# Optimization experiments

Measured on AMD Instinct MI355X. Metric: run time of the kernel, lower is better.

Reference implementation:

```python
import jax, jax.numpy as jnp
import numpy as np

H = 256           # hidden_size
S = 4             # num_subspaces
D = H // S        # subspace dim = 64
HD = 64           # mLSTM head_dim
EPS = 1e-8


def setup_inputs() -> dict:
    key = jax.random.key(0)
    ks = iter(jax.random.split(key, 40))
    def w(shape, scale=0.02):
        return (jax.random.normal(next(ks), shape, dtype=jnp.float32) * scale)
    B, T, Din = 256, 512, 128
    inp = {
        'x': jax.random.normal(next(ks), (B, T, Din), dtype=jnp.float32),
        # input projection
        'W_in': w((Din, H)), 'b_in': jnp.zeros((H,), jnp.float32),
        # layer 0: sLSTM (forget_bias buffer is zeros -> folded into b? keep explicit)
        's0_Wih': w((H, 4 * H)), 's0_bih': jnp.zeros((4 * H,), jnp.float32),
        's0_Whh': w((H, 4 * H)),
        # layer 1: mLSTM
        'm_Wq': w((H, HD)), 'm_bq': jnp.zeros((HD,), jnp.float32),
        'm_Wk': w((H, HD)), 'm_bk': jnp.zeros((HD,), jnp.float32),
        'm_Wv': w((H, HD)), 'm_bv': jnp.zeros((HD,), jnp.float32),
        'm_Wi': w((H, 1)), 'm_bi': jnp.zeros((1,), jnp.float32),
        'm_Wf': w((H, 1)), 'm_bf': jnp.zeros((1,), jnp.float32),
        'm_Wo': w((H, H)), 'm_bo': jnp.zeros((H,), jnp.float32),
        'm_Wp': w((HD, H)), 'm_bp': jnp.zeros((H,), jnp.float32),
        # subspace sLSTM cells (stacked over S); forget bias = -log(2^s)
        'sub_Wih': w((S, D, 4 * D)), 'sub_bih': jnp.zeros((S, 4 * D), jnp.float32),
        'sub_Whh': w((S, D, 4 * D)),
        'sub_fbias': jnp.asarray(-np.log(2.0 ** np.arange(S)), jnp.float32)[:, None] * jnp.ones((S, D), jnp.float32),
        # memory attention MLP
        'att_W1': w((D, D)), 'att_b1': jnp.zeros((D,), jnp.float32),
        'att_W2': w((D, 1)), 'att_b2': jnp.zeros((1,), jnp.float32),
        # layer norm
        'ln_g': jnp.ones((H,), jnp.float32), 'ln_b': jnp.zeros((H,), jnp.float32),
    }
    return inp


def _forward(x, W_in, b_in, s0_Wih, s0_bih, s0_Whh,
             m_Wq, m_bq, m_Wk, m_bk, m_Wv, m_bv, m_Wi, m_bi, m_Wf, m_bf,
             m_Wo, m_bo, m_Wp, m_bp,
             sub_Wih, sub_bih, sub_Whh, sub_fbias,
             att_W1, att_b1, att_W2, att_b2, ln_g, ln_b):
    B, T, _ = x.shape
    xh = x @ W_in + b_in                      # [B,T,H]
    xh = jnp.swapaxes(xh, 0, 1)               # [T,B,H] for scan

    def slstm(xt, h, c, n, Wih, bih, Whh, fbias):
        gates = xt @ Wih + bih + h @ Whh
        ig, fg, og, ct = jnp.split(gates, 4, axis=-1)
        i = jnp.exp(ig)
        f = jax.nn.sigmoid(fg + fbias)
        o = jax.nn.sigmoid(og)
        c_new = f * c + i * jnp.tanh(ct)
        n_new = f * n + i
        h_new = o * jnp.tanh(c_new / (n_new + EPS))
        return h_new, c_new, n_new

    def step(carry, xt):
        (h0, c0, n0, C1, n1, hs, cs, ns, _) = carry
        # layer 0: sLSTM, residual
        h0n, c0n, n0n = slstm(xt, h0, c0, n0, s0_Wih, s0_bih, s0_Whh, 0.0)
        x1 = h0n + xt
        # layer 1: mLSTM, residual
        q = x1 @ m_Wq + m_bq
        k = x1 @ m_Wk + m_bk
        v = x1 @ m_Wv + m_bv
        i1 = jnp.exp(x1 @ m_Wi + m_bi)              # [B,1]
        f1 = jax.nn.sigmoid(x1 @ m_Wf + m_bf)       # [B,1]
        C1n = f1[:, :, None] * C1 + i1[:, :, None] * (v[:, :, None] * k[:, None, :])
        n1n = f1 * n1 + i1                          # [B,1]
        Cq = jnp.einsum('bij,bj->bi', C1n, q)       # [B,HD]
        h_tilde = Cq / (n1n + EPS)
        o1 = jax.nn.sigmoid(x1 @ m_Wo + m_bo)
        h1n = o1 * jnp.tanh(h_tilde @ m_Wp + m_bp)
        x2 = h1n + x1
        # subspace sLSTM cells over S chunks (vectorized over s)
        xs = jnp.swapaxes(x2.reshape(B, S, D), 0, 1)   # [S,B,D]
        gates = (jnp.einsum('sbd,sdg->sbg', xs, sub_Wih) + sub_bih[:, None, :]
                 + jnp.einsum('sbd,sdg->sbg', hs, sub_Whh))
        ig, fg, og, ct = jnp.split(gates, 4, axis=-1)
        i = jnp.exp(ig)
        f = jax.nn.sigmoid(fg + sub_fbias[:, None, :])
        o = jax.nn.sigmoid(og)
        csn = f * cs + i * jnp.tanh(ct)
        nsn = f * ns + i
        hsn = o * jnp.tanh(csn / (nsn + EPS))          # [S,B,D]
        # attention fusion across subspaces
        score = jnp.tanh(hsn @ att_W1 + att_b1) @ att_W2 + att_b2  # [S,B,1]
        w = jax.nn.softmax(score[..., 0], axis=0)                  # [S,B]
        h_fused = jnp.sum(w[:, :, None] * hsn, axis=0)             # [B,D]
        h_final = jnp.tile(h_fused, (1, S))                        # [B,H]
        return (h0n, c0n, n0n, C1n, n1n, hsn, csn, nsn, h_final), None

    z = jnp.zeros
    carry0 = (z((B, H)), z((B, H)), jnp.ones((B, H)),
              z((B, HD, HD)), jnp.ones((B, 1)),
              z((S, B, D)), z((S, B, D)), jnp.ones((S, B, D)),
              z((B, H)))
    carryT, _ = jax.lax.scan(step, carry0, xh)
    out = carryT[-1]                                 # last-step h_final [B,H]
    mu = jnp.mean(out, axis=-1, keepdims=True)
    var = jnp.mean((out - mu) ** 2, axis=-1, keepdims=True)
    return (out - mu) / jnp.sqrt(var + 1e-5) * ln_g + ln_b


def reference(x, W_in, b_in, s0_Wih, s0_bih, s0_Whh,
              m_Wq, m_bq, m_Wk, m_bk, m_Wv, m_bv, m_Wi, m_bi, m_Wf, m_bf,
              m_Wo, m_bo, m_Wp, m_bp,
              sub_Wih, sub_bih, sub_Whh, sub_fbias,
              att_W1, att_b1, att_W2, att_b2, ln_g, ln_b):
    return _forward(x, W_in, b_in, s0_Wih, s0_bih, s0_Whh,
                    m_Wq, m_bq, m_Wk, m_bk, m_Wv, m_bv, m_Wi, m_bi, m_Wf, m_bf,
                    m_Wo, m_bo, m_Wp, m_bp,
                    sub_Wih, sub_bih, sub_Whh, sub_fbias,
                    att_W1, att_b1, att_W2, att_b2, ln_g, ln_b)
```

## Files before the change

### kernel.cpp

```cpp
#include <hip/hip_runtime.h>
#include <math.h>

#define TSTEPS 512
#define CH 16
#define NCHUNK 32
#define EPSR 1e-8f

#define OHH   0u
#define OSUB  262144u
#define OQK   393216u
#define OV    425984u
#define OWO   442368u
#define OWP   507904u
#define OWIN  524288u
#define NPACK1 557056u
#define OWC   557056u
#define OBC   688128u

typedef __fp16 h2_t __attribute__((ext_vector_type(2)));

__device__ __forceinline__ float dot2(unsigned int w, unsigned int a, float acc) {
    union U { unsigned int u; h2_t h; };
    U cw; cw.u = w; U ca; ca.u = a;
    return __builtin_amdgcn_fdot2(cw.h, ca.h, acc, false);
}
__device__ __forceinline__ unsigned int pk2f(float a, float b) {
    union { h2_t h; unsigned int u; } c;
    c.h = __builtin_amdgcn_cvt_pkrtz(a, b);
    return c.u;
}
__device__ __forceinline__ float bfu(unsigned int v) {
    union { unsigned int i; float f; } c; c.i = v; return c.f;
}
__device__ __forceinline__ float sigmoidf_(float v) { return 1.0f / (1.0f + expf(-v)); }
__device__ __forceinline__ unsigned short f2bf(float f) {
    unsigned int u = __float_as_uint(f);
    return (unsigned short)((u + 0x7fffu + ((u >> 16) & 1u)) >> 16);
}

extern "C" __global__ void pack_w(const float* __restrict__ Whh,
    const float* __restrict__ sWih, const float* __restrict__ sWhh,
    const float* __restrict__ Wq, const float* __restrict__ Wk, const float* __restrict__ Wv,
    const float* __restrict__ Wo, const float* __restrict__ Wp,
    const float* __restrict__ W_in, unsigned short* __restrict__ ws)
{
    unsigned e = blockIdx.x * 256u + threadIdx.x;
    if (e >= NPACK1) return;
    float v; bool isbf = false;
    if (e < OSUB) {
        unsigned idx = e >> 3, sl = e & 7u;
        unsigned jp = idx >> 8, t = idx & 255u, g = sl >> 1, ee = sl & 1u;
        v = Whh[(2u * jp + ee) * 1024u + g * 256u + t];
    } else if (e < OQK) {
        unsigned r = e - OSUB, idx = r >> 3, sl = r & 7u;
        unsigned q4 = idx & 3u, d = (idx >> 2) & 63u, jq = (idx >> 8) & 15u, s = idx >> 12;
        unsigned g = sl >> 1, ee = sl & 1u;
        unsigned j = jq * 4u + (q4 & 1u) * 2u + ee;
        const float* src = (q4 >> 1) ? sWhh : sWih;
        v = src[(s * 64u + j) * 256u + g * 64u + d];
    } else if (e < OV) {
        unsigned r = e - OQK, idx = r >> 3, sl = r & 7u;
        unsigned d = idx & 63u, jq = idx >> 6;
        unsigned j = jq * 4u + (sl & 3u);
        v = ((sl >> 2) ? Wk : Wq)[j * 64u + d];
    } else if (e < OWO) {
        unsigned r = e - OV, idx = r >> 2;
        unsigned d = idx & 63u, jq = idx >> 6, j = jq * 4u + (r & 3u);
        v = Wv[j * 64u + d];
    } else if (e < OWP) {
        unsigned r = e - OWO, idx = r >> 2;
        unsigned t = idx & 255u, jq = idx >> 8, j = jq * 4u + (r & 3u);
        v = Wo[j * 256u + t];
    } else if (e < OWIN) {
        unsigned r = e - OWP, idx = r >> 2;
        unsigned t = idx & 255u, jq = idx >> 8, j = jq * 4u + (r & 3u);
        v = Wp[j * 256u + t];
    } else {
        v = W_in[e - OWIN]; isbf = true;
    }
    if (isbf) ws[e] = f2bf(v);
    else { union { __fp16 h; unsigned short s; } c; c.h = (__fp16)v; ws[e] = c.s; }
}

extern "C" __global__ void compute_wc(const float* __restrict__ W_in,
    const float* __restrict__ Wih, const float* __restrict__ b_in,
    const float* __restrict__ bih, unsigned short* __restrict__ ws)
{
    unsigned e = blockIdx.x * 256u + threadIdx.x;
    if (e < 131072u) {
        unsigned k = e >> 10, n = e & 1023u;
        float acc = 0.f;
        for (int j = 0; j < 256; ++j) acc += W_in[k * 256 + j] * Wih[j * 1024 + n];
        unsigned t = n & 255u, g = n >> 8;
        ws[OWC + k * 1024 + t * 4 + g] = f2bf(acc);
    } else if (e < 132096u) {
        unsigned n = e - 131072u;
        float acc = bih[n];
        for (int j = 0; j < 256; ++j) acc += b_in[j] * Wih[j * 1024 + n];
        float* bc = (float*)(ws + OBC);
        bc[n] = acc;
    }
}

extern "C" __global__ __launch_bounds__(512)
void xlstm_seq(const float* __restrict__ x, const float* __restrict__ b_in,
               const float* __restrict__ bq, const float* __restrict__ bk, const float* __restrict__ bv,
               const float* __restrict__ Wi, const float* __restrict__ bi,
               const float* __restrict__ Wf, const float* __restrict__ bf,
               const float* __restrict__ bo, const float* __restrict__ bp,
               const float* __restrict__ sbih, const float* __restrict__ sfb,
               const float* __restrict__ aW1, const float* __restrict__ ab1,
               const float* __restrict__ aW2, const float* __restrict__ ab2,
               const float* __restrict__ lng, const float* __restrict__ lnb,
               const unsigned short* __restrict__ pk,
               float* __restrict__ out)
{
    const int u = threadIdx.x;
    const int b = blockIdx.x;
    const int t256 = u & 255;
    const int half = u >> 8;

    __shared__ float g_chunk[CH][1024];
    __shared__ float xt_chunk[CH][256];
    __shared__ __align__(16) float xT[128][20];
    __shared__ __align__(16) float x1_l[256], hs_l[256];
    __shared__ float opre_l[256];
    __shared__ float psum[4][520];
    __shared__ float qb[64], kb[64], vb[64];
    __shared__ float Cm[64 * 65];
    __shared__ float sc_l[16];
    __shared__ __align__(16) float Wi_l[256], Wf_l[256];
    __shared__ float sbih_l[1024], bc_l[1024];
    __shared__ float b_in_l[256], bo_l[256], bp_l[256], sfb_l[256], bqkv_l[192];
    __shared__ __align__(16) unsigned int h0p[128], x1p[128], x2p[128], hsp[128], htp[32];

    {
        const float* bcg = (const float*)(pk + OBC);
        for (int e = u; e < 1024; e += 512) { sbih_l[e] = sbih[e]; bc_l[e] = bcg[e]; }
    }
    if (u < 256) {
        Wi_l[u] = Wi[u]; Wf_l[u] = Wf[u];
        b_in_l[u] = b_in[u]; bo_l[u] = bo[u]; bp_l[u] = bp[u]; sfb_l[u] = sfb[u];
        hs_l[u] = 0.f;
    }
    if (u < 192) bqkv_l[u] = (u < 64) ? bq[u] : (u < 128) ? bk[u - 64] : bv[u - 128];
    if (u < 128) { h0p[u] = 0u; hsp[u] = 0u; }
    if (u == 0) { sc_l[10] = bi[0]; sc_l[11] = bf[0]; }
    for (int e = u; e < 64 * 65; e += 512) Cm[e] = 0.f;
    float c0 = 0.f, n0 = 1.f, cs = 0.f, ns = 1.f, n1 = 1.f;
    __syncthreads();

    const uint4* pwhh = reinterpret_cast<const uint4*>(pk + OHH) + t256;
    const uint4* psub = reinterpret_cast<const uint4*>(pk + OSUB)
                        + ((size_t)((t256 >> 6) * 1024 + (t256 & 63))) * 4;
    const uint4* pqk = reinterpret_cast<const uint4*>(pk + OQK) + (u & 63);
    const uint2* pv_ = reinterpret_cast<const uint2*>(pk + OV) + (u & 63);
    const uint2* pwo = reinterpret_cast<const uint2*>(pk + OWO) + t256;
    const uint2* pwp = reinterpret_cast<const uint2*>(pk + OWP) + t256;
    const unsigned short* pwin = pk + OWIN + t256;
    const uint2* pwc = reinterpret_cast<const uint2*>(pk + OWC) + t256;
    const float* xrow = x + (size_t)b * TSTEPS * 128;

    for (int cc = 0; cc < NCHUNK; ++cc) {
        {
            float4 xv4 = *reinterpret_cast<const float4*>(xrow + cc * (CH * 128) + u * 4);
            int m = u >> 5, k0 = (u * 4) & 127;
            xT[k0][m] = xv4.x; xT[k0 + 1][m] = xv4.y; xT[k0 + 2][m] = xv4.z; xT[k0 + 3][m] = xv4.w;
        }
        __syncthreads();

        {
            const int m0 = half * 8;
            float xtacc[8], gacc[4][8];
            {
                float bi_ = b_in_l[t256];
                #pragma unroll
                for (int e = 0; e < 8; ++e) xtacc[e] = bi_;
                #pragma unroll
                for (int g = 0; g < 4; ++g) {
                    float bcv = bc_l[g * 256 + t256];
                    #pragma unroll
                    for (int e = 0; e < 8; ++e) gacc[g][e] = bcv;
                }
            }
            #pragma unroll 4
            for (int k = 0; k < 128; ++k) {
                float wv = bfu((unsigned)pwin[k * 256] << 16);
                uint2 wg = pwc[k * 256];
                float w0 = bfu(wg.x << 16), w1 = bfu(wg.x & 0xffff0000u);
                float w2 = bfu(wg.y << 16), w3 = bfu(wg.y & 0xffff0000u);
                float4 a  = *reinterpret_cast<const float4*>(&xT[k][m0]);
                float4 b4 = *reinterpret_cast<const float4*>(&xT[k][m0 + 4]);
                #pragma unroll
                for (int e = 0; e < 8; ++e) {
                    float xv = (e == 0) ? a.x : (e == 1) ? a.y : (e == 2) ? a.z : (e == 3) ? a.w
                             : (e == 4) ? b4.x : (e == 5) ? b4.y : (e == 6) ? b4.z : b4.w;
                    xtacc[e]   += xv * wv;
                    gacc[0][e] += xv * w0;
                    gacc[1][e] += xv * w1;
                    gacc[2][e] += xv * w2;
                    gacc[3][e] += xv * w3;
                }
            }
            #pragma unroll
            for (int e = 0; e < 8; ++e) {
                xt_chunk[m0 + e][t256] = xtacc[e];
                g_chunk[m0 + e][t256]       = gacc[0][e];
                g_chunk[m0 + e][256 + t256] = gacc[1][e];
                g_chunk[m0 + e][512 + t256] = gacc[2][e];
                g_chunk[m0 + e][768 + t256] = gacc[3][e];
            }
        }
        __syncthreads();

        for (int st = 0; st < CH; ++st) {
            {
                float g0 = 0.f, g1 = 0.f, g2 = 0.f, g3 = 0.f;
                const int jp0 = half * 64;
                #pragma unroll 4
                for (int q = 0; q < 16; ++q) {
                    uint4 hp4 = *reinterpret_cast<const uint4*>(&h0p[jp0 + q * 4]);
                    #pragma unroll
                    for (int e = 0; e < 4; ++e) {
                        uint4 wk = pwhh[(size_t)(jp0 + q * 4 + e) * 256];
                        unsigned int hp = (e == 0) ? hp4.x : (e == 1) ? hp4.y : (e == 2) ? hp4.z : hp4.w;
                        g0 = dot2(wk.x, hp, g0);
                        g1 = dot2(wk.y, hp, g1);
                        g2 = dot2(wk.z, hp, g2);
                        g3 = dot2(wk.w, hp, g3);
                    }
                }
                psum[0][u] = g0; psum[1][u] = g1; psum[2][u] = g2; psum[3][u] = g3;
            }
            __syncthreads();
            if (u < 256) {
                float G0 = g_chunk[st][u]       + psum[0][u] + psum[0][256 + u];
                float G1 = g_chunk[st][256 + u] + psum[1][u] + psum[1][256 + u];
                float G2 = g_chunk[st][512 + u] + psum[2][u] + psum[2][256 + u];
                float G3 = g_chunk[st][768 + u] + psum[3][u] + psum[3][256 + u];
                float i0 = expf(G0), f0 = sigmoidf_(G1), o0 = sigmoidf_(G2);
                float cn = f0 * c0 + i0 * tanhf(G3);
                float nn = f0 * n0 + i0;
                c0 = cn; n0 = nn;
                float h0n = o0 * tanhf(cn / (nn + EPSR));
                float x1v = h0n + xt_chunk[st][u];
                x1_l[u] = x1v;
                float h0o = __shfl_xor(h0n, 1);
                float x1o = __shfl_xor(x1v, 1);
                if (!(u & 1)) { h0p[u >> 1] = pk2f(h0n, h0o); x1p[u >> 1] = pk2f(x1v, x1o); }
            }
            __syncthreads();

            if (u < 256) {
                const int jq0 = (u >> 6) * 16;
                float pq = 0.f, pkk = 0.f, pvv = 0.f;
                #pragma unroll 4
                for (int q = 0; q < 16; ++q) {
                    int jq = jq0 + q;
                    uint4 wqk = pqk[(size_t)jq * 64];
                    uint2 wv2 = pv_[(size_t)jq * 64];
                    uint2 ap = *reinterpret_cast<const uint2*>(&x1p[jq * 2]);
                    pq  = dot2(wqk.x, ap.x, pq);  pq  = dot2(wqk.y, ap.y, pq);
                    pkk = dot2(wqk.z, ap.x, pkk); pkk = dot2(wqk.w, ap.y, pkk);
                    pvv = dot2(wv2.x, ap.x, pvv); pvv = dot2(wv2.y, ap.y, pvv);
                }
                psum[0][u] = pq; psum[1][u] = pkk; psum[2][u] = pvv;
            } else if (u < 384) {
                const float* Wl = (u < 320) ? Wi_l : Wf_l;
                int j0 = (u & 63) * 4;
                float4 xv = *reinterpret_cast<const float4*>(&x1_l[j0]);
                float4 wv = *reinterpret_cast<const float4*>(&Wl[j0]);
                float p = xv.x * wv.x + xv.y * wv.y + xv.z * wv.z + xv.w * wv.w;
                #pragma unroll
                for (int off = 32; off > 0; off >>= 1) p += __shfl_down(p, off);
                if ((u & 63) == 0) sc_l[(u < 320) ? 8 : 9] = p;
            }
            __syncthreads();
            {
                int lane = u & 63;
                if (u < 64)        qb[u]    = bqkv_l[u]          + psum[0][u] + psum[0][64 + u] + psum[0][128 + u] + psum[0][192 + u];
                else if (u < 128)  kb[lane] = bqkv_l[64 + lane]  + psum[1][lane] + psum[1][64 + lane] + psum[1][128 + lane] + psum[1][192 + lane];
                else if (u < 192)  vb[lane] = bqkv_l[128 + lane] + psum[2][lane] + psum[2][64 + lane] + psum[2][128 + lane] + psum[2][192 + lane];
                else if (u == 192) sc_l[0] = expf(sc_l[10] + sc_l[8]);
                else if (u == 193) sc_l[1] = sigmoidf_(sc_l[11] + sc_l[9]);
            }
            __syncthreads();

            float i1 = sc_l[0], f1 = sc_l[1];
            n1 = f1 * n1 + i1;
            {
                int r = u >> 3, ci = (u & 7) * 8;
                float vi = i1 * vb[r];
                float cqp = 0.f;
                #pragma unroll
                for (int e = 0; e < 8; ++e) {
                    int c = ci + e;
                    float cmv = f1 * Cm[r * 65 + c] + vi * kb[c];
                    Cm[r * 65 + c] = cmv;
                    cqp += cmv * qb[c];
                }
                cqp += __shfl_down(cqp, 4);
                cqp += __shfl_down(cqp, 2);
                cqp += __shfl_down(cqp, 1);
                float htv = cqp / (n1 + EPSR);
                float hto = __shfl_xor(htv, 8);
                if ((u & 15) == 0) htp[u >> 4] = pk2f(htv, hto);

                float p = 0.f;
                const int jq0 = half * 32;
                #pragma unroll 4
                for (int q = 0; q < 32; ++q) {
                    int jq = jq0 + q;
                    uint2 w2 = pwo[(size_t)jq * 256];
                    uint2 ap = *reinterpret_cast<const uint2*>(&x1p[jq * 2]);
                    p = dot2(w2.x, ap.x, p); p = dot2(w2.y, ap.y, p);
                }
                psum[3][u] = p;
            }
            __syncthreads();

            {
                if (u < 256) opre_l[u] = bo_l[u] + psum[3][u] + psum[3][256 + u];
                float p = 0.f;
                const int jq0 = half * 8;
                #pragma unroll
                for (int q = 0; q < 8; ++q) {
                    int jq = jq0 + q;
                    uint2 w2 = pwp[(size_t)jq * 256];
                    uint2 ap = *reinterpret_cast<const uint2*>(&htp[jq * 2]);
                    p = dot2(w2.x, ap.x, p); p = dot2(w2.y, ap.y, p);
                }
                psum[0][u] = p;
            }
            __syncthreads();
            if (u < 256) {
                float pp = bp_l[u] + psum[0][u] + psum[0][256 + u];
                float h1 = sigmoidf_(opre_l[u]) * tanhf(pp);
                float x2v = h1 + x1_l[u];
                float x2o = __shfl_xor(x2v, 1);
                if (!(u & 1)) x2p[u >> 1] = pk2f(x2v, x2o);
            }
            __syncthreads();

            {
                const int sbase = (t256 >> 6) * 32;
                const int jqb = half * 8;
                float g0 = 0.f, g1 = 0.f, g2 = 0.f, g3 = 0.f;
                #pragma unroll 2
                for (int q = 0; q < 8; ++q) {
                    int jq = jqb + q;
                    const uint4* pp4 = psub + (size_t)jq * 256;
                    uint4 wih0 = pp4[0], wih1 = pp4[1], whh0 = pp4[2], whh1 = pp4[3];
                    uint2 xp = *reinterpret_cast<const uint2*>(&x2p[sbase + jq * 2]);
                    uint2 hp = *reinterpret_cast<const uint2*>(&hsp[sbase + jq * 2]);
                    g0 = dot2(wih0.x, xp.x, g0); g0 = dot2(wih1.x, xp.y, g0);
                    g0 = dot2(whh0.x, hp.x, g0); g0 = dot2(whh1.x, hp.y, g0);
                    g1 = dot2(wih0.y, xp.x, g1); g1 = dot2(wih1.y, xp.y, g1);
                    g1 = dot2(whh0.y, hp.x, g1); g1 = dot2(whh1.y, hp.y, g1);
                    g2 = dot2(wih0.z, xp.x, g2); g2 = dot2(wih1.z, xp.y, g2);
                    g2 = dot2(whh0.z, hp.x, g2); g2 = dot2(whh1.z, hp.y, g2);
                    g3 = dot2(wih0.w, xp.x, g3); g3 = dot2(wih1.w, xp.y, g3);
                    g3 = dot2(whh0.w, hp.x, g3); g3 = dot2(whh1.w, hp.y, g3);
                }
                psum[0][u] = g0; psum[1][u] = g1; psum[2][u] = g2; psum[3][u] = g3;
            }
            __syncthreads();
            if (u < 256) {
                int s = u >> 6, dd = u & 63;
                float sg0 = psum[0][u] + psum[0][256 + u] + sbih_l[s * 256 + dd];
                float sg1 = psum[1][u] + psum[1][256 + u] + sbih_l[s * 256 + 64 + dd];
                float sg2 = psum[2][u] + psum[2][256 + u] + sbih_l[s * 256 + 128 + dd];
                float sg3 = psum[3][u] + psum[3][256 + u] + sbih_l[s * 256 + 192 + dd];
                float si = expf(sg0);
                float sf = sigmoidf_(sg1 + sfb_l[u]);
                float so = sigmoidf_(sg2);
                float csn = sf * cs + si * tanhf(sg3);
                float nsn = sf * ns + si;
                cs = csn; ns = nsn;
                float hsn = so * tanhf(csn / (nsn + EPSR));
                hs_l[u] = hsn;
                float hso = __shfl_xor(hsn, 1);
                if (!(u & 1)) hsp[u >> 1] = pk2f(hsn, hso);
            }
            __syncthreads();
        }
    }

    if (u < 256) {
        int s = u >> 6, dd = u & 63;
        float av = ab1[dd];
        for (int j = 0; j < 64; ++j) av += hs_l[s * 64 + j] * aW1[j * 64 + dd];
        float contrib = tanhf(av) * aW2[dd];
        #pragma unroll
        for (int off = 32; off > 0; off >>= 1) contrib += __shfl_down(contrib, off);
        if (dd == 0) sc_l[4 + s] = contrib + ab2[0];
    }
    __syncthreads();
    if (u < 256) {
        float a0 = sc_l[4], a1 = sc_l[5], a2 = sc_l[6], a3 = sc_l[7];
        float m = fmaxf(fmaxf(a0, a1), fmaxf(a2, a3));
        float e0 = expf(a0 - m), e1 = expf(a1 - m), e2 = expf(a2 - m), e3 = expf(a3 - m);
        float inv = 1.f / (e0 + e1 + e2 + e3);
        int dd = u & 63;
        psum[0][u] = (e0 * hs_l[dd] + e1 * hs_l[64 + dd] + e2 * hs_l[128 + dd] + e3 * hs_l[192 + dd]) * inv;
    }
    __syncthreads();
    if (u < 256) {
        float mu = 0.f;
        for (int j = 0; j < 256; ++j) mu += psum[0][j];
        mu *= (1.0f / 256.0f);
        float var = 0.f;
        for (int j = 0; j < 256; ++j) { float dv = psum[0][j] - mu; var += dv * dv; }
        var *= (1.0f / 256.0f);
        out[b * 256 + u] = (psum[0][u] - mu) / sqrtf(var + 1e-5f) * lng[u] + lnb[u];
    }
}

extern "C" void kernel_launch(void* const* d_in, const int* in_sizes, int n_in,
                              void* d_out, int out_size, void* d_ws, size_t ws_size,
                              hipStream_t stream) {
    (void)in_sizes; (void)n_in; (void)out_size; (void)ws_size;
    const float* x     = (const float*)d_in[0];
    const float* W_in  = (const float*)d_in[1];
    const float* b_in  = (const float*)d_in[2];
    const float* Wih   = (const float*)d_in[3];
    const float* bih   = (const float*)d_in[4];
    const float* Whh   = (const float*)d_in[5];
    const float* Wq    = (const float*)d_in[6];
    const float* bq    = (const float*)d_in[7];
    const float* Wk    = (const float*)d_in[8];
    const float* bk    = (const float*)d_in[9];
    const float* Wv    = (const float*)d_in[10];
    const float* bv    = (const float*)d_in[11];
    const float* Wi    = (const float*)d_in[12];
    const float* bi    = (const float*)d_in[13];
    const float* Wf    = (const float*)d_in[14];
    const float* bf    = (const float*)d_in[15];
    const float* Wo    = (const float*)d_in[16];
    const float* bo    = (const float*)d_in[17];
    const float* Wp    = (const float*)d_in[18];
    const float* bp    = (const float*)d_in[19];
    const float* sWih  = (const float*)d_in[20];
    const float* sbih  = (const float*)d_in[21];
    const float* sWhh  = (const float*)d_in[22];
    const float* sfb   = (const float*)d_in[23];
    const float* aW1   = (const float*)d_in[24];
    const float* ab1   = (const float*)d_in[25];
    const float* aW2   = (const float*)d_in[26];
    const float* ab2   = (const float*)d_in[27];
    const float* lng   = (const float*)d_in[28];
    const float* lnb   = (const float*)d_in[29];
    float* out = (float*)d_out;
    unsigned short* ws = (unsigned short*)d_ws;

    pack_w<<<dim3((NPACK1 + 255u) / 256u), dim3(256), 0, stream>>>(
        Whh, sWih, sWhh, Wq, Wk, Wv, Wo, Wp, W_in, ws);
    compute_wc<<<dim3(517), dim3(256), 0, stream>>>(W_in, Wih, b_in, bih, ws);

    xlstm_seq<<<dim3(256), dim3(512), 0, stream>>>(
        x, b_in, bq, bk, bv, Wi, bi, Wf, bf, bo, bp,
        sbih, sfb, aW1, ab1, aW2, ab2, lng, lnb, ws, out);
}
```

Baseline: 7.102 ms.

## Pack two batch rows per 1024-thread block with fp16 chunk staging

The sequence kernel now handles two batch elements per workgroup of 1024 threads, 128 blocks instead of 256. Each half runs the same per-step recurrence on its own shared-memory state, so weight reads from L2/L1 are shared between the two rows. The chunk size is halved and the precomputed gate and input-projection chunks are kept in fp16 to fit the duplicated shared memory. The cost is that only 128 of the 256 CUs are used, barriers now cover 1024 threads, and the fp16 staging adds rounding error to the gate inputs.

Result: slower. 13.65 ms (+92.2%).

```diff
diff --git a/kernel.cpp b/kernel.cpp
--- a/kernel.cpp
+++ b/kernel.cpp
@@ -2,8 +2,8 @@
 #include <math.h>
 
 #define TSTEPS 512
-#define CH 16
-#define NCHUNK 32
+#define CH 8
+#define NCHUNK 64
 #define EPSR 1e-8f
 
 #define OHH   0u
@@ -28,6 +28,12 @@
     union { h2_t h; unsigned int u; } c;
     c.h = __builtin_amdgcn_cvt_pkrtz(a, b);
     return c.u;
+}
+__device__ __forceinline__ unsigned short f2h(float f) {
+    union { __fp16 h; unsigned short s; } c; c.h = (__fp16)f; return c.s;
+}
+__device__ __forceinline__ float h2f(unsigned short s) {
+    union { unsigned short s; __fp16 h; } c; c.s = s; return (float)c.h;
 }
 __device__ __forceinline__ float bfu(unsigned int v) {
     union { unsigned int i; float f; } c; c.i = v; return c.f;
@@ -79,7 +85,7 @@
         v = W_in[e - OWIN]; isbf = true;
     }
     if (isbf) ws[e] = f2bf(v);
-    else { union { __fp16 h; unsigned short s; } c; c.h = (__fp16)v; ws[e] = c.s; }
+    else ws[e] = f2h(v);
 }
 
 extern "C" __global__ void compute_wc(const float* __restrict__ W_in,
@@ -102,7 +108,7 @@
     }
 }
 
-extern "C" __global__ __launch_bounds__(512)
+extern "C" __global__ __launch_bounds__(1024)
 void xlstm_seq(const float* __restrict__ x, const float* __restrict__ b_in,
                const float* __restrict__ bq, const float* __restrict__ bk, const float* __restrict__ bv,
                const float* __restrict__ Wi, const float* __restrict__ bi,
@@ -116,71 +122,71 @@
                float* __restrict__ out)
 {
     const int u = threadIdx.x;
-    const int b = blockIdx.x;
-    const int t256 = u & 255;
-    const int half = u >> 8;
-
-    __shared__ float g_chunk[CH][1024];
-    __shared__ float xt_chunk[CH][256];
-    __shared__ __align__(16) float xT[128][20];
-    __shared__ __align__(16) float x1_l[256], hs_l[256];
-    __shared__ float opre_l[256];
-    __shared__ float psum[4][520];
-    __shared__ float qb[64], kb[64], vb[64];
-    __shared__ float Cm[64 * 65];
-    __shared__ float sc_l[16];
+    const int g = u >> 9;
+    const int v = u & 511;
+    const int t256 = v & 255;
+    const int half = v >> 8;
+
+    __shared__ unsigned short g_chunk[2][CH][1024];
+    __shared__ unsigned short xt_chunk[2][CH][256];
+    __shared__ __align__(16) float xT[2][128][12];
+    __shared__ __align__(16) float x1_l[2][256], hs_l[2][256];
+    __shared__ float psum[2][4][520];
+    __shared__ float qb[2][64], kb[2][64], vb[2][64];
+    __shared__ float Cm[2][64 * 65];
+    __shared__ float sc_l[2][16];
     __shared__ __align__(16) float Wi_l[256], Wf_l[256];
     __shared__ float sbih_l[1024], bc_l[1024];
     __shared__ float b_in_l[256], bo_l[256], bp_l[256], sfb_l[256], bqkv_l[192];
-    __shared__ __align__(16) unsigned int h0p[128], x1p[128], x2p[128], hsp[128], htp[32];
+    __shared__ __align__(8) unsigned int h0p[2][128], x1p[2][128], x2p[2][128], hsp[2][128], htp[2][32];
 
     {
         const float* bcg = (const float*)(pk + OBC);
-        for (int e = u; e < 1024; e += 512) { sbih_l[e] = sbih[e]; bc_l[e] = bcg[e]; }
+        if (u < 1024) { sbih_l[u] = sbih[u]; bc_l[u] = bcg[u]; }
     }
     if (u < 256) {
         Wi_l[u] = Wi[u]; Wf_l[u] = Wf[u];
         b_in_l[u] = b_in[u]; bo_l[u] = bo[u]; bp_l[u] = bp[u]; sfb_l[u] = sfb[u];
-        hs_l[u] = 0.f;
     }
     if (u < 192) bqkv_l[u] = (u < 64) ? bq[u] : (u < 128) ? bk[u - 64] : bv[u - 128];
-    if (u < 128) { h0p[u] = 0u; hsp[u] = 0u; }
-    if (u == 0) { sc_l[10] = bi[0]; sc_l[11] = bf[0]; }
-    for (int e = u; e < 64 * 65; e += 512) Cm[e] = 0.f;
+    if (v < 256) hs_l[g][v] = 0.f;
+    if (v < 128) { h0p[g][v] = 0u; hsp[g][v] = 0u; }
+    if (v == 0) { sc_l[g][10] = bi[0]; sc_l[g][11] = bf[0]; }
+    for (int e = v; e < 64 * 65; e += 512) Cm[g][e] = 0.f;
     float c0 = 0.f, n0 = 1.f, cs = 0.f, ns = 1.f, n1 = 1.f;
     __syncthreads();
 
     const uint4* pwhh = reinterpret_cast<const uint4*>(pk + OHH) + t256;
     const uint4* psub = reinterpret_cast<const uint4*>(pk + OSUB)
                         + ((size_t)((t256 >> 6) * 1024 + (t256 & 63))) * 4;
-    const uint4* pqk = reinterpret_cast<const uint4*>(pk + OQK) + (u & 63);
-    const uint2* pv_ = reinterpret_cast<const uint2*>(pk + OV) + (u & 63);
+    const uint4* pqk = reinterpret_cast<const uint4*>(pk + OQK) + (v & 63);
+    const uint2* pv_ = reinterpret_cast<const uint2*>(pk + OV) + (v & 63);
     const uint2* pwo = reinterpret_cast<const uint2*>(pk + OWO) + t256;
     const uint2* pwp = reinterpret_cast<const uint2*>(pk + OWP) + t256;
     const unsigned short* pwin = pk + OWIN + t256;
     const uint2* pwc = reinterpret_cast<const uint2*>(pk + OWC) + t256;
-    const float* xrow = x + (size_t)b * TSTEPS * 128;
+    const float* xrow = x + (size_t)(blockIdx.x * 2 + g) * TSTEPS * 128;
 
     for (int cc = 0; cc < NCHUNK; ++cc) {
         {
-            float4 xv4 = *reinterpret_cast<const float4*>(xrow + cc * (CH * 128) + u * 4);
-            int m = u >> 5, k0 = (u * 4) & 127;
-            xT[k0][m] = xv4.x; xT[k0 + 1][m] = xv4.y; xT[k0 + 2][m] = xv4.z; xT[k0 + 3][m] = xv4.w;
+            float2 xv2 = *reinterpret_cast<const float2*>(xrow + cc * (CH * 128) + v * 2);
+            int m = v >> 6, k0 = (v * 2) & 127;
+            xT[g][k0][m] = xv2.x; xT[g][k0 + 1][m] = xv2.y;
         }
         __syncthreads();
 
         {
-            const int m0 = half * 8;
-            float xtacc[8], gacc[4][8];
+            const int m0 = half * 4;
+            float xtacc[4], gacc[4][4];
             {
                 float bi_ = b_in_l[t256];
                 #pragma unroll
-                for (int e = 0; e < 8; ++e) xtacc[e] = bi_;
-                #pragma unroll
-                for (int g = 0; g < 4; ++g) {
-                    float bcv = bc_l[g * 256 + t256];
+                for (int e = 0; e < 4; ++e) xtacc[e] = bi_;
+                #pragma unroll
+                for (int q = 0; q < 4; ++q) {
+                    float bcv = bc_l[q * 256 + t256];
                     #pragma unroll
-                    for (int e = 0; e < 8; ++e) gacc[g][e] = bcv;
+                    for (int e = 0; e < 4; ++e) gacc[q][e] = bcv;
                 }
             }
             #pragma unroll 4
@@ -189,12 +195,10 @@
                 uint2 wg = pwc[k * 256];
                 float w0 = bfu(wg.x << 16), w1 = bfu(wg.x & 0xffff0000u);
                 float w2 = bfu(wg.y << 16), w3 = bfu(wg.y & 0xffff0000u);
-                float4 a  = *reinterpret_cast<const float4*>(&xT[k][m0]);
-                float4 b4 = *reinterpret_cast<const float4*>(&xT[k][m0 + 4]);
-                #pragma unroll
-                for (int e = 0; e < 8; ++e) {
-                    float xv = (e == 0) ? a.x : (e == 1) ? a.y : (e == 2) ? a.z : (e == 3) ? a.w
-                             : (e == 4) ? b4.x : (e == 5) ? b4.y : (e == 6) ? b4.z : b4.w;
+                float4 a = *reinterpret_cast<const float4*>(&xT[g][k][m0]);
+                #pragma unroll
+                for (int e = 0; e < 4; ++e) {
+                    float xv = (e == 0) ? a.x : (e == 1) ? a.y : (e == 2) ? a.z : a.w;
                     xtacc[e]   += xv * wv;
                     gacc[0][e] += xv * w0;
                     gacc[1][e] += xv * w1;
@@ -203,12 +207,12 @@
                 }
             }
             #pragma unroll
-            for (int e = 0; e < 8; ++e) {
-                xt_chunk[m0 + e][t256] = xtacc[e];
-                g_chunk[m0 + e][t256]       = gacc[0][e];
-                g_chunk[m0 + e][256 + t256] = gacc[1][e];
-                g_chunk[m0 + e][512 + t256] = gacc[2][e];
-                g_chunk[m0 + e][768 + t256] = gacc[3][e];
+            for (int e = 0; e < 4; ++e) {
+                xt_chunk[g][m0 + e][t256] = f2h(xtacc[e]);
+                g_chunk[g][m0 + e][t256]       = f2h(gacc[0][e]);
+                g_chunk[g][m0 + e][256 + t256] = f2h(gacc[1][e]);
+                g_chunk[g][m0 + e][512 + t256] = f2h(gacc[2][e]);
+                g_chunk[g][m0 + e][768 + t256] = f2h(gacc[3][e]);
             }
         }
         __syncthreads();
@@ -219,7 +223,7 @@
                 const int jp0 = half * 64;
                 #pragma unroll 4
                 for (int q = 0; q < 16; ++q) {
-                    uint4 hp4 = *reinterpret_cast<const uint4*>(&h0p[jp0 + q * 4]);
+                    uint4 hp4 = *reinterpret_cast<const uint4*>(&h0p[g][jp0 + q * 4]);
                     #pragma unroll
                     for (int e = 0; e < 4; ++e) {
                         uint4 wk = pwhh[(size_t)(jp0 + q * 4 + e) * 256];
@@ -230,81 +234,81 @@
                         g3 = dot2(wk.w, hp, g3);
                     }
                 }
-                psum[0][u] = g0; psum[1][u] = g1; psum[2][u] = g2; psum[3][u] = g3;
-            }
-            __syncthreads();
-            if (u < 256) {
-                float G0 = g_chunk[st][u]       + psum[0][u] + psum[0][256 + u];
-                float G1 = g_chunk[st][256 + u] + psum[1][u] + psum[1][256 + u];
-                float G2 = g_chunk[st][512 + u] + psum[2][u] + psum[2][256 + u];
-                float G3 = g_chunk[st][768 + u] + psum[3][u] + psum[3][256 + u];
+                psum[g][0][v] = g0; psum[g][1][v] = g1; psum[g][2][v] = g2; psum[g][3][v] = g3;
+            }
+            __syncthreads();
+            if (v < 256) {
+                float G0 = h2f(g_chunk[g][st][v])       + psum[g][0][v] + psum[g][0][256 + v];
+                float G1 = h2f(g_chunk[g][st][256 + v]) + psum[g][1][v] + psum[g][1][256 + v];
+                float G2 = h2f(g_chunk[g][st][512 + v]) + psum[g][2][v] + psum[g][2][256 + v];
+                float G3 = h2f(g_chunk[g][st][768 + v]) + psum[g][3][v] + psum[g][3][256 + v];
                 float i0 = expf(G0), f0 = sigmoidf_(G1), o0 = sigmoidf_(G2);
                 float cn = f0 * c0 + i0 * tanhf(G3);
                 float nn = f0 * n0 + i0;
                 c0 = cn; n0 = nn;
                 float h0n = o0 * tanhf(cn / (nn + EPSR));
-                float x1v = h0n + xt_chunk[st][u];
-                x1_l[u] = x1v;
+                float x1v = h0n + h2f(xt_chunk[g][st][v]);
+                x1_l[g][v] = x1v;
                 float h0o = __shfl_xor(h0n, 1);
                 float x1o = __shfl_xor(x1v, 1);
-                if (!(u & 1)) { h0p[u >> 1] = pk2f(h0n, h0o); x1p[u >> 1] = pk2f(x1v, x1o); }
-            }
-            __syncthreads();
-
-            if (u < 256) {
-                const int jq0 = (u >> 6) * 16;
+                if (!(v & 1)) { h0p[g][v >> 1] = pk2f(h0n, h0o); x1p[g][v >> 1] = pk2f(x1v, x1o); }
+            }
+            __syncthreads();
+
+            if (v < 256) {
+                const int jq0 = (v >> 6) * 16;
                 float pq = 0.f, pkk = 0.f, pvv = 0.f;
                 #pragma unroll 4
                 for (int q = 0; q < 16; ++q) {
                     int jq = jq0 + q;
                     uint4 wqk = pqk[(size_t)jq * 64];
                     uint2 wv2 = pv_[(size_t)jq * 64];
-                    uint2 ap = *reinterpret_cast<const uint2*>(&x1p[jq * 2]);
+                    uint2 ap = *reinterpret_cast<const uint2*>(&x1p[g][jq * 2]);
                     pq  = dot2(wqk.x, ap.x, pq);  pq  = dot2(wqk.y, ap.y, pq);
                     pkk = dot2(wqk.z, ap.x, pkk); pkk = dot2(wqk.w, ap.y, pkk);
                     pvv = dot2(wv2.x, ap.x, pvv); pvv = dot2(wv2.y, ap.y, pvv);
                 }
-                psum[0][u] = pq; psum[1][u] = pkk; psum[2][u] = pvv;
-            } else if (u < 384) {
-                const float* Wl = (u < 320) ? Wi_l : Wf_l;
-                int j0 = (u & 63) * 4;
-                float4 xv = *reinterpret_cast<const float4*>(&x1_l[j0]);
+                psum[g][0][v] = pq; psum[g][1][v] = pkk; psum[g][2][v] = pvv;
+            } else if (v < 384) {
+                const float* Wl = (v < 320) ? Wi_l : Wf_l;
+                int j0 = (v & 63) * 4;
+                float4 xv = *reinterpret_cast<const float4*>(&x1_l[g][j0]);
                 float4 wv = *reinterpret_cast<const float4*>(&Wl[j0]);
                 float p = xv.x * wv.x + xv.y * wv.y + xv.z * wv.z + xv.w * wv.w;
                 #pragma unroll
                 for (int off = 32; off > 0; off >>= 1) p += __shfl_down(p, off);
-                if ((u & 63) == 0) sc_l[(u < 320) ? 8 : 9] = p;
-            }
-            __syncthreads();
-            {
-                int lane = u & 63;
-                if (u < 64)        qb[u]    = bqkv_l[u]          + psum[0][u] + psum[0][64 + u] + psum[0][128 + u] + psum[0][192 + u];
-                else if (u < 128)  kb[lane] = bqkv_l[64 + lane]  + psum[1][lane] + psum[1][64 + lane] + psum[1][128 + lane] + psum[1][192 + lane];
-                else if (u < 192)  vb[lane] = bqkv_l[128 + lane] + psum[2][lane] + psum[2][64 + lane] + psum[2][128 + lane] + psum[2][192 + lane];
-                else if (u == 192) sc_l[0] = expf(sc_l[10] + sc_l[8]);
-                else if (u == 193) sc_l[1] = sigmoidf_(sc_l[11] + sc_l[9]);
-            }
-            __syncthreads();
-
-            float i1 = sc_l[0], f1 = sc_l[1];
+                if ((v & 63) == 0) sc_l[g][(v < 320) ? 8 : 9] = p;
+            }
+            __syncthreads();
+            {
+                int lane = v & 63;
+                if (v < 64)        qb[g][v]    = bqkv_l[v]          + psum[g][0][v] + psum[g][0][64 + v] + psum[g][0][128 + v] + psum[g][0][192 + v];
+                else if (v < 128)  kb[g][lane] = bqkv_l[64 + lane]  + psum[g][1][lane] + psum[g][1][64 + lane] + psum[g][1][128 + lane] + psum[g][1][192 + lane];
+                else if (v < 192)  vb[g][lane] = bqkv_l[128 + lane] + psum[g][2][lane] + psum[g][2][64 + lane] + psum[g][2][128 + lane] + psum[g][2][192 + lane];
+                else if (v == 192) sc_l[g][0] = expf(sc_l[g][10] + sc_l[g][8]);
+                else if (v == 193) sc_l[g][1] = sigmoidf_(sc_l[g][11] + sc_l[g][9]);
+            }
+            __syncthreads();
+
+            float i1 = sc_l[g][0], f1 = sc_l[g][1];
             n1 = f1 * n1 + i1;
             {
-                int r = u >> 3, ci = (u & 7) * 8;
-                float vi = i1 * vb[r];
+                int r = v >> 3, ci = (v & 7) * 8;
+                float vi = i1 * vb[g][r];
                 float cqp = 0.f;
                 #pragma unroll
                 for (int e = 0; e < 8; ++e) {
                     int c = ci + e;
-                    float cmv = f1 * Cm[r * 65 + c] + vi * kb[c];
-                    Cm[r * 65 + c] = cmv;
-                    cqp += cmv * qb[c];
+                    float cmv = f1 * Cm[g][r * 65 + c] + vi * kb[g][c];
+                    Cm[g][r * 65 + c] = cmv;
+                    cqp += cmv * qb[g][c];
                 }
                 cqp += __shfl_down(cqp, 4);
                 cqp += __shfl_down(cqp, 2);
                 cqp += __shfl_down(cqp, 1);
                 float htv = cqp / (n1 + EPSR);
                 float hto = __shfl_xor(htv, 8);
-                if ((u & 15) == 0) htp[u >> 4] = pk2f(htv, hto);
+                if ((v & 15) == 0) htp[g][v >> 4] = pk2f(htv, hto);
 
                 float p = 0.f;
                 const int jq0 = half * 32;
@@ -312,33 +316,33 @@
                 for (int q = 0; q < 32; ++q) {
                     int jq = jq0 + q;
                     uint2 w2 = pwo[(size_t)jq * 256];
-                    uint2 ap = *reinterpret_cast<const uint2*>(&x1p[jq * 2]);
+                    uint2 ap = *reinterpret_cast<const uint2*>(&x1p[g][jq * 2]);
                     p = dot2(w2.x, ap.x, p); p = dot2(w2.y, ap.y, p);
                 }
-                psum[3][u] = p;
-            }
-            __syncthreads();
-
-            {
-                if (u < 256) opre_l[u] = bo_l[u] + psum[3][u] + psum[3][256 + u];
+                psum[g][3][v] = p;
+            }
+            __syncthreads();
+
+            {
                 float p = 0.f;
                 const int jq0 = half * 8;
                 #pragma unroll
                 for (int q = 0; q < 8; ++q) {
                     int jq = jq0 + q;
                     uint2 w2 = pwp[(size_t)jq * 256];
-                    uint2 ap = *reinterpret_cast<const uint2*>(&htp[jq * 2]);
+                    uint2 ap = *reinterpret_cast<const uint2*>(&htp[g][jq * 2]);
                     p = dot2(w2.x, ap.x, p); p = dot2(w2.y, ap.y, p);
                 }
-                psum[0][u] = p;
-            }
-            __syncthreads();
-            if (u < 256) {
-                float pp = bp_l[u] + psum[0][u] + psum[0][256 + u];
-                float h1 = sigmoidf_(opre_l[u]) * tanhf(pp);
-                float x2v = h1 + x1_l[u];
+                psum[g][0][v] = p;
+            }
+            __syncthreads();
+            if (v < 256) {
+                float opre = bo_l[v] + psum[g][3][v] + psum[g][3][256 + v];
+                float pp = bp_l[v] + psum[g][0][v] + psum[g][0][256 + v];
+                float h1 = sigmoidf_(opre) * tanhf(pp);
+                float x2v = h1 + x1_l[g][v];
                 float x2o = __shfl_xor(x2v, 1);
-                if (!(u & 1)) x2p[u >> 1] = pk2f(x2v, x2o);
+                if (!(v & 1)) x2p[g][v >> 1] = pk2f(x2v, x2o);
             }
             __syncthreads();
 
@@ -351,8 +355,8 @@
                     int jq = jqb + q;
                     const uint4* pp4 = psub + (size_t)jq * 256;
                     uint4 wih0 = pp4[0], wih1 = pp4[1], whh0 = pp4[2], whh1 = pp4[3];
-                    uint2 xp = *reinterpret_cast<const uint2*>(&x2p[sbase + jq * 2]);
-                    uint2 hp = *reinterpret_cast<const uint2*>(&hsp[sbase + jq * 2]);
+                    uint2 xp = *reinterpret_cast<const uint2*>(&x2p[g][sbase + jq * 2]);
+                    uint2 hp = *reinterpret_cast<const uint2*>(&hsp[g][sbase + jq * 2]);
                     g0 = dot2(wih0.x, xp.x, g0); g0 = dot2(wih1.x, xp.y, g0);
                     g0 = dot2(whh0.x, hp.x, g0); g0 = dot2(whh1.x, hp.y, g0);
                     g1 = dot2(wih0.y, xp.x, g1); g1 = dot2(wih1.y, xp.y, g1);
@@ -362,57 +366,57 @@
                     g3 = dot2(wih0.w, xp.x, g3); g3 = dot2(wih1.w, xp.y, g3);
                     g3 = dot2(whh0.w, hp.x, g3); g3 = dot2(whh1.w, hp.y, g3);
                 }
-                psum[0][u] = g0; psum[1][u] = g1; psum[2][u] = g2; psum[3][u] = g3;
-            }
-            __syncthreads();
-            if (u < 256) {
-                int s = u >> 6, dd = u & 63;
-                float sg0 = psum[0][u] + psum[0][256 + u] + sbih_l[s * 256 + dd];
-                float sg1 = psum[1][u] + psum[1][256 + u] + sbih_l[s * 256 + 64 + dd];
-                float sg2 = psum[2][u] + psum[2][256 + u] + sbih_l[s * 256 + 128 + dd];
-                float sg3 = psum[3][u] + psum[3][256 + u] + sbih_l[s * 256 + 192 + dd];
+                psum[g][0][v] = g0; psum[g][1][v] = g1; psum[g][2][v] = g2; psum[g][3][v] = g3;
+            }
+            __syncthreads();
+            if (v < 256) {
+                int s = v >> 6, dd = v & 63;
+                float sg0 = psum[g][0][v] + psum[g][0][256 + v] + sbih_l[s * 256 + dd];
+                float sg1 = psum[g][1][v] + psum[g][1][256 + v] + sbih_l[s * 256 + 64 + dd];
+                float sg2 = psum[g][2][v] + psum[g][2][256 + v] + sbih_l[s * 256 + 128 + dd];
+                float sg3 = psum[g][3][v] + psum[g][3][256 + v] + sbih_l[s * 256 + 192 + dd];
                 float si = expf(sg0);
-                float sf = sigmoidf_(sg1 + sfb_l[u]);
+                float sf = sigmoidf_(sg1 + sfb_l[v]);
                 float so = sigmoidf_(sg2);
                 float csn = sf * cs + si * tanhf(sg3);
                 float nsn = sf * ns + si;
                 cs = csn; ns = nsn;
                 float hsn = so * tanhf(csn / (nsn + EPSR));
-                hs_l[u] = hsn;
+                hs_l[g][v] = hsn;
                 float hso = __shfl_xor(hsn, 1);
-                if (!(u & 1)) hsp[u >> 1] = pk2f(hsn, hso);
+                if (!(v & 1)) hsp[g][v >> 1] = pk2f(hsn, hso);
             }
             __syncthreads();
         }
     }
 
-    if (u < 256) {
-        int s = u >> 6, dd = u & 63;
+    if (v < 256) {
+        int s = v >> 6, dd = v & 63;
         float av = ab1[dd];
-        for (int j = 0; j < 64; ++j) av += hs_l[s * 64 + j] * aW1[j * 64 + dd];
+        for (int j = 0; j < 64; ++j) av += hs_l[g][s * 64 + j] * aW1[j * 64 + dd];
         float contrib = tanhf(av) * aW2[dd];
         #pragma unroll
         for (int off = 32; off > 0; off >>= 1) contrib += __shfl_down(contrib, off);
-        if (dd == 0) sc_l[4 + s] = contrib + ab2[0];
+        if (dd == 0) sc_l[g][4 + s] = contrib + ab2[0];
     }
     __syncthreads();
-    if (u < 256) {
-        float a0 = sc_l[4], a1 = sc_l[5], a2 = sc_l[6], a3 = sc_l[7];
+    if (v < 256) {
+        float a0 = sc_l[g][4], a1 = sc_l[g][5], a2 = sc_l[g][6], a3 = sc_l[g][7];
         float m = fmaxf(fmaxf(a0, a1), fmaxf(a2, a3));
         float e0 = expf(a0 - m), e1 = expf(a1 - m), e2 = expf(a2 - m), e3 = expf(a3 - m);
         float inv = 1.f / (e0 + e1 + e2 + e3);
-        int dd = u & 63;
-        psum[0][u] = (e0 * hs_l[dd] + e1 * hs_l[64 + dd] + e2 * hs_l[128 + dd] + e3 * hs_l[192 + dd]) * inv;
+        int dd = v & 63;
+        psum[g][0][v] = (e0 * hs_l[g][dd] + e1 * hs_l[g][64 + dd] + e2 * hs_l[g][128 + dd] + e3 * hs_l[g][192 + dd]) * inv;
     }
     __syncthreads();
-    if (u < 256) {
+    if (v < 256) {
         float mu = 0.f;
-        for (int j = 0; j < 256; ++j) mu += psum[0][j];
+        for (int j = 0; j < 256; ++j) mu += psum[g][0][j];
         mu *= (1.0f / 256.0f);
         float var = 0.f;
-        for (int j = 0; j < 256; ++j) { float dv = psum[0][j] - mu; var += dv * dv; }
+        for (int j = 0; j < 256; ++j) { float dv = psum[g][0][j] - mu; var += dv * dv; }
         var *= (1.0f / 256.0f);
-        out[b * 256 + u] = (psum[0][u] - mu) / sqrtf(var + 1e-5f) * lng[u] + lnb[u];
+        out[(size_t)(blockIdx.x * 2 + g) * 256 + v] = (psum[g][0][v] - mu) / sqrtf(var + 1e-5f) * lng[v] + lnb[v];
     }
 }
 
@@ -457,7 +461,7 @@
         Whh, sWih, sWhh, Wq, Wk, Wv, Wo, Wp, W_in, ws);
     compute_wc<<<dim3(517), dim3(256), 0, stream>>>(W_in, Wih, b_in, bih, ws);
 
-    xlstm_seq<<<dim3(256), dim3(512), 0, stream>>>(
+    xlstm_seq<<<dim3(128), dim3(1024), 0, stream>>>(
         x, b_in, bq, bk, bv, Wi, bi, Wf, bf, bo, bp,
         sbih, sfb, aW1, ab1, aW2, ab2, lng, lnb, ws, out);
 }
```
